# Kernel tuning notes

Hardware: AMD Instinct MI355X
Metric: run time of the kernel (lower is better)

Reference implementation:

```python
import jax, jax.numpy as jnp
import numpy as np

B, F, D, V = 8192, 26, 32, 100000
H1, H2 = 128, 128  # cin_size
U1, U2 = 400, 400  # dnn hidden units


def setup_inputs() -> dict:
    key = jax.random.key(0)
    ks = jax.random.split(key, 12)
    s = 0.05  # keep activations/sigmoid in a sane range
    return {
        "dense_inputs": jax.random.normal(ks[0], (B, 13), jnp.float32),
        "sparse_inputs": jax.random.randint(ks[1], (B, F), 0, V, jnp.int32),
        "E": jax.random.normal(ks[2], (F, V, D), jnp.float32) * s,
        "W_cin0": jax.random.normal(ks[3], (F, F, H1), jnp.float32) * s,
        "W_cin1": jax.random.normal(ks[4], (F, H1, H2), jnp.float32) * s,
        "W1": jax.random.normal(ks[5], (F * D, U1), jnp.float32) * s,
        "b1": jnp.zeros((U1,), jnp.float32),
        "W2": jax.random.normal(ks[6], (U1, U2), jnp.float32) * s,
        "b2": jnp.zeros((U2,), jnp.float32),
        "w_lin": jax.random.normal(ks[7], (F, 1), jnp.float32) * s,
        "b_lin": jnp.zeros((1,), jnp.float32),
        "w_out": jax.random.normal(ks[8], (1 + H1 + H2 + U2 + 13, 1), jnp.float32) * s,
        "b_out": jnp.zeros((1,), jnp.float32),
    }


def reference(dense_inputs, sparse_inputs, E, W_cin0, W_cin1, W1, b1, W2, b2,
              w_lin, b_lin, w_out, b_out):
    # Linear part: Dense(1) applied to raw (cast) sparse ids, as in the TF code.
    linear_out = sparse_inputs.astype(jnp.float32) @ w_lin + b_lin  # [B,1]

    # Embedding lookup: per-field tables. embed[b,f,:] = E[f, sparse[b,f], :]
    embed = E[jnp.arange(F)[None, :], sparse_inputs]  # [B,F,D]

    # CIN. The split->matmul->reshape->conv1d chain is exactly:
    #   x_{k+1}[b,h,d] = sum_{i,j} W_k[i,j,h] * X0[b,i,d] * x_k[b,j,d]
    X0 = embed
    x1 = jnp.einsum('bid,bjd,ijh->bhd', X0, X0, W_cin0)   # [B,H1,D]
    x2 = jnp.einsum('bid,bjd,ijh->bhd', X0, x1, W_cin1)   # [B,H2,D]
    cin_out = jnp.concatenate([x1, x2], axis=1).sum(axis=-1)  # [B,H1+H2]

    # DNN on flattened embeddings (dropout rate 0 -> identity at inference).
    v = embed.reshape(B, F * D)
    h = jax.nn.relu(v @ W1 + b1)
    h = jax.nn.relu(h @ W2 + b2)  # [B,U2]

    total = jnp.concatenate([linear_out, cin_out, h, dense_inputs], axis=-1)
    return jax.nn.sigmoid(total @ w_out + b_out)  # [B,1]
```

## Files before the change

kernel.cpp:

```cpp
#include <hip/hip_runtime.h>
#include <hip/hip_bf16.h>
#include <math.h>

typedef __attribute__((ext_vector_type(8))) short bf16x8;
typedef __attribute__((ext_vector_type(4))) float f32x4;

#define B_ 8192
#define F_ 26
#define D_ 32
#define V_ 100000
#define NP_ 351
#define KP_ 352

static const size_t OFF_VB   = 0;
static const size_t OFF_FD0  = 13631488;
static const size_t OFF_PDH2 = 13664256;
static const size_t OFF_H1B  = 13795328;
static const size_t OFF_W0T  = 20348928;
static const size_t OFF_W1T  = 20439040;
static const size_t OFF_W2T  = 21104640;
static const size_t OFF_MWT  = 21424640;

static __device__ __forceinline__ unsigned short f2b(float f) {
    unsigned int u = __float_as_uint(f);
    return (unsigned short)((u + 0x7FFF + ((u >> 16) & 1)) >> 16);
}
static __device__ __forceinline__ unsigned short f2bt(float f) {
    return (unsigned short)(__float_as_uint(f) >> 16);
}
static __device__ __forceinline__ unsigned int pk2t(float a, float b) {
    return __builtin_amdgcn_perm(__float_as_uint(b), __float_as_uint(a), 0x07060302u);
}
static __device__ __forceinline__ float bf2f(unsigned short u) {
    return __uint_as_float(((unsigned int)u) << 16);
}

static __device__ __forceinline__ void transpose_body(
    const float* __restrict__ src, unsigned short* __restrict__ dst,
    int K, int N, int bx, int by)
{
    __shared__ float tl[32][33];
    const int lx = threadIdx.x & 31, ly = threadIdx.x >> 5;
    const int n0 = bx * 32, k0 = by * 32;
#pragma unroll
    for (int i = 0; i < 4; ++i) {
        int k = k0 + ly + i * 8, n = n0 + lx;
        if (k < K && n < N) tl[ly + i * 8][lx] = src[(size_t)k * N + n];
    }
    __syncthreads();
#pragma unroll
    for (int i = 0; i < 4; ++i) {
        int n = n0 + ly + i * 8, k = k0 + lx;
        if (k < K && n < N) dst[(size_t)n * K + k] = f2b(tl[lx][ly + i * 8]);
    }
}

__global__ __launch_bounds__(256) void k0_all(
    const float* __restrict__ W0, const float* __restrict__ Wc1,
    const float* __restrict__ W1, const float* __restrict__ W2,
    const float* __restrict__ wout,
    unsigned short* __restrict__ W0t, unsigned short* __restrict__ W1t,
    unsigned short* __restrict__ W2t, float* __restrict__ Mwt)
{
    int bid = blockIdx.x;
    if (bid < 176) {
        int g = bid * 256 + threadIdx.x;
        if (g < 128 * KP_) {
            int h = g / KP_, p = g % KP_;
            float w = 0.f;
            if (p < NP_) {
                int i = 0, base = 0;
                while (base + (F_ - i) <= p) { base += F_ - i; ++i; }
                int j = i + (p - base);
                w = W0[(i * F_ + j) * 128 + h];
                if (i != j) w += W0[(j * F_ + i) * 128 + h];
            }
            W0t[g] = f2b(w);
        }
        return;
    }
    bid -= 176;
    if (bid < 338) { transpose_body(W1, W1t, 832, 400, bid % 13, bid / 13); return; }
    bid -= 338;
    if (bid < 169) { transpose_body(W2, W2t, 400, 400, bid % 13, bid / 13); return; }
    bid -= 169;
    {
        int g = bid * 256 + threadIdx.x;
        if (g < 128 * 32) {
            int j = g >> 5, i = g & 31;
            float s = 0.f;
            if (i < F_) {
                const float* row = Wc1 + ((size_t)i * 128 + j) * 128;
                for (int h = 0; h < 128; ++h) s = fmaf(row[h], wout[129 + h], s);
            }
            Mwt[g] = s;
        }
    }
}

__global__ __launch_bounds__(256) void k1_embed_cin(
    const int*   __restrict__ sparse,
    const float* __restrict__ E,
    const unsigned short* __restrict__ W0t,
    const float* __restrict__ wlin,
    const float* __restrict__ blin,
    const float* __restrict__ wout,
    const float* __restrict__ Mwt,
    unsigned short* __restrict__ vb,
    float* __restrict__ fdot0)
{
    __shared__ __align__(16) unsigned short embB[64][40];
    __shared__ __align__(16) unsigned short Pbuf[64 * 360];
    __shared__ float wdot[4];
    __shared__ float linv[52];
    __shared__ int   idxs[52];
    __shared__ unsigned char pI[NP_], pJ[NP_];

    const int b0 = blockIdx.x * 2, t = threadIdx.x;

    if (t < 52) {
        int bb = t >= 26 ? 1 : 0, ff = t - bb * 26;
        int id = sparse[(b0 + bb) * F_ + ff];
        idxs[t] = id;
        linv[t] = (float)id * wlin[ff];
    }
    if (t < F_) {
        int i = t, base = F_ * i - (i * (i - 1)) / 2;
        for (int j = i; j < F_; ++j) { pI[base + j - i] = (unsigned char)i; pJ[base + j - i] = (unsigned char)j; }
    }
    __syncthreads();

    for (int r = t; r < 416; r += 256) {
        int f = r >> 3, q = r & 7;
        int bb = f >= 26 ? 1 : 0, ff = f - bb * 26;
        float4 v4 = *(const float4*)(E + ((size_t)ff * V_ + idxs[f]) * D_ + q * 4);
        uint2 uu; uu.x = pk2t(v4.x, v4.y); uu.y = pk2t(v4.z, v4.w);
        *(uint2*)&embB[bb * 32 + ff][q * 4] = uu;
        *(uint2*)(vb + (size_t)(b0 + bb) * 832 + ff * 32 + q * 4) = uu;
    }
    if (t < 192) {
        int row = t >> 4, bb = row >= 6 ? 1 : 0, rr = row - bb * 6;
        *(unsigned int*)&embB[bb * 32 + 26 + rr][(t & 15) * 2] = 0u;
    }
    __syncthreads();

    {
        const int d = t & 31, sub = t >> 5;
        const int bb = sub & 1, pb = sub >> 1;
        const int e0 = bb * 32;
        const int p0 = pb * 88;
        unsigned short* Prow = &Pbuf[(e0 + d) * 360];
        for (int k = 0; k < 44; ++k) {
            int p = p0 + 2 * k;
            float a = bf2f(embB[e0 + pI[p]][d]) * bf2f(embB[e0 + pJ[p]][d]);
            float c = (p + 1 < NP_) ? bf2f(embB[e0 + pI[p + 1]][d]) * bf2f(embB[e0 + pJ[p + 1]][d]) : 0.f;
            *(unsigned int*)&Prow[p] = pk2t(a, c);
        }
    }
    __syncthreads();

    const int wave = t >> 6, lane = t & 63;
    const int lr = lane & 15, lg = lane >> 4;
    const int bb = wave & 1;
    const int h0 = (wave >> 1) * 64;
    f32x4 acc[2][4] = {};
    {
        const unsigned short* Ab = &Pbuf[(bb * 32 + lr) * 360];
        const unsigned short* Bb = W0t + (size_t)(h0 + lr) * KP_ + lg * 8;
        for (int kt = 0; kt < 11; ++kt) {
            const int ko = kt * 32 + lg * 8;
            bf16x8 a0 = *(const bf16x8*)(Ab + ko);
            bf16x8 a1 = *(const bf16x8*)(Ab + 16 * 360 + ko);
#pragma unroll
            for (int n = 0; n < 4; ++n) {
                bf16x8 bw = *(const bf16x8*)(Bb + (size_t)(n * 16) * KP_ + kt * 32);
                acc[0][n] = __builtin_amdgcn_mfma_f32_16x16x32_bf16(a0, bw, acc[0][n], 0, 0, 0);
                acc[1][n] = __builtin_amdgcn_mfma_f32_16x16x32_bf16(a1, bw, acc[1][n], 0, 0, 0);
            }
        }
    }

    float dotv = 0.f;
#pragma unroll
    for (int n = 0; n < 4; ++n) {
        float s = acc[0][n][0] + acc[0][n][1] + acc[0][n][2] + acc[0][n][3]
                + acc[1][n][0] + acc[1][n][1] + acc[1][n][2] + acc[1][n][3];
        s += __shfl_xor(s, 16, 64);
        s += __shfl_xor(s, 32, 64);
        if (lg == 0) dotv += s * wout[1 + h0 + n * 16 + lr];
    }
    __syncthreads();

#pragma unroll
    for (int n = 0; n < 4; ++n) {
        const int base = ((bb << 7) + h0 + n * 16 + lr) * 40;
#pragma unroll
        for (int mi = 0; mi < 2; ++mi) {
            *(unsigned int*)&Pbuf[base + mi * 16 + lg * 4]     = pk2t(acc[mi][n][0], acc[mi][n][1]);
            *(unsigned int*)&Pbuf[base + mi * 16 + lg * 4 + 2] = pk2t(acc[mi][n][2], acc[mi][n][3]);
        }
    }
    __syncthreads();

    {
        bf16x8 ga0 = *(const bf16x8*)&embB[bb * 32 + lr][lg * 8];
        bf16x8 ga1 = *(const bf16x8*)&embB[bb * 32 + 16 + lr][lg * 8];
#pragma unroll
        for (int n = 0; n < 4; ++n) {
            const int j = h0 + n * 16 + lr;
            bf16x8 xb = *(const bf16x8*)&Pbuf[((bb << 7) + j) * 40 + lg * 8];
            f32x4 g0 = {}, g1 = {};
            g0 = __builtin_amdgcn_mfma_f32_16x16x32_bf16(ga0, xb, g0, 0, 0, 0);
            g1 = __builtin_amdgcn_mfma_f32_16x16x32_bf16(ga1, xb, g1, 0, 0, 0);
            const float* mr = Mwt + j * 32;
            float4 m0 = *(const float4*)(mr + lg * 4);
            float4 m1 = *(const float4*)(mr + 16 + lg * 4);
            dotv += g0[0] * m0.x + g0[1] * m0.y + g0[2] * m0.z + g0[3] * m0.w
                  + g1[0] * m1.x + g1[1] * m1.y + g1[2] * m1.z + g1[3] * m1.w;
        }
    }
#pragma unroll
    for (int off = 1; off <= 32; off <<= 1) dotv += __shfl_xor(dotv, off, 64);
    if (lane == 0) wdot[wave] = dotv;
    __syncthreads();

    if (t < 2) {
        float s = blin[0];
        for (int f = 0; f < F_; ++f) s += linv[t * 26 + f];
        fdot0[b0 + t] = s * wout[0] + wdot[t] + wdot[t + 2];
    }
}

static __device__ __forceinline__ void gemm_core(
    const unsigned short* __restrict__ A, int lda,
    const unsigned short* __restrict__ Bt, int ldb, int N,
    int m0, int n0, int kbase, int kend,
    unsigned short (*As)[40], unsigned short (*Bs)[40],
    f32x4 (*acc)[2])
{
    const int t = threadIdx.x;
    const int wave = t >> 6, lane = t & 63;
    const int lr = lane & 15, lg = lane >> 4;
    const int wn = wave * 32;
    const int ar = t >> 2, kg = (t & 3) * 8;

    const unsigned short* aptr = A  + (size_t)(m0 + ar) * lda + kbase + kg;
    const unsigned short* bp0  = Bt + (size_t)(n0 + ar) * ldb + kbase + kg;
    const unsigned short* bp1  = Bt + (size_t)(n0 + 64 + ar) * ldb + kbase + kg;
    const bool bn0 = (n0 + ar) < N, bn1 = (n0 + 64 + ar) < N;
    const uint4 z4 = make_uint4(0u, 0u, 0u, 0u);
    const int nkt = (kend - kbase + 31) >> 5;
    uint4 av, bv0, bv1;
    {
        int k = kbase + kg;
        av  = (k < kend)        ? *(const uint4*)aptr : z4;
        bv0 = (bn0 && k < kend) ? *(const uint4*)bp0  : z4;
        bv1 = (bn1 && k < kend) ? *(const uint4*)bp1  : z4;
    }
    for (int kt = 0; kt < nkt; ++kt) {
        *(uint4*)&As[ar][kg]      = av;
        *(uint4*)&Bs[ar][kg]      = bv0;
        *(uint4*)&Bs[64 + ar][kg] = bv1;
        __syncthreads();
        if (kt + 1 < nkt) {
            int kn = kbase + (kt + 1) * 32 + kg;
            av  = (kn < kend)        ? *(const uint4*)(aptr + (kt + 1) * 32) : z4;
            bv0 = (bn0 && kn < kend) ? *(const uint4*)(bp0  + (kt + 1) * 32) : z4;
            bv1 = (bn1 && kn < kend) ? *(const uint4*)(bp1  + (kt + 1) * 32) : z4;
        }
        bf16x8 af[4], bfr[2];
#pragma unroll
        for (int i = 0; i < 4; ++i) af[i]  = *(const bf16x8*)&As[i * 16 + lr][lg * 8];
#pragma unroll
        for (int j = 0; j < 2; ++j) bfr[j] = *(const bf16x8*)&Bs[wn + j * 16 + lr][lg * 8];
#pragma unroll
        for (int i = 0; i < 4; ++i)
#pragma unroll
            for (int j = 0; j < 2; ++j)
                acc[i][j] = __builtin_amdgcn_mfma_f32_16x16x32_bf16(af[i], bfr[j], acc[i][j], 0, 0, 0);
        __syncthreads();
    }
}

__global__ __launch_bounds__(256) void k2_h1(
    const unsigned short* __restrict__ vb, const unsigned short* __restrict__ W1t,
    const float* __restrict__ b1, unsigned short* __restrict__ h1b)
{
    __shared__ __align__(16) unsigned short As[64][40];
    __shared__ __align__(16) unsigned short Bs[128][40];
    const int t = threadIdx.x;
    const int wave = t >> 6, lane = t & 63;
    const int lr = lane & 15, lg = lane >> 4;
    const int m0 = blockIdx.y * 64, n0 = blockIdx.x * 128;
    f32x4 acc[4][2] = {};
    gemm_core(vb, 832, W1t, 832, 400, m0, n0, 0, 832, As, Bs, acc);
#pragma unroll
    for (int i = 0; i < 4; ++i) {
        int mrow = m0 + i * 16 + lg * 4;
#pragma unroll
        for (int j = 0; j < 2; ++j) {
            int col = n0 + wave * 32 + j * 16 + lr;
            if (col >= 400) continue;
            float bb = b1[col];
#pragma unroll
            for (int r = 0; r < 4; ++r)
                h1b[(size_t)(mrow + r) * 400 + col] = f2bt(fmaxf(acc[i][j][r] + bb, 0.f));
        }
    }
}

__global__ __launch_bounds__(256) void k2_h2(
    const unsigned short* __restrict__ h1b, const unsigned short* __restrict__ W2t,
    const float* __restrict__ b2, const float* __restrict__ wout,
    float* __restrict__ pdh2)
{
    __shared__ __align__(16) unsigned short As[64][40];
    __shared__ __align__(16) unsigned short Bs[128][40];
    __shared__ float red[4][64];
    const int t = threadIdx.x;
    const int wave = t >> 6, lane = t & 63;
    const int lr = lane & 15, lg = lane >> 4;
    const int m0 = blockIdx.y * 64, n0 = blockIdx.x * 128;
    f32x4 acc[4][2] = {};
    gemm_core(h1b, 400, W2t, 400, 400, m0, n0, 0, 400, As, Bs, acc);
    float v[4][4];
#pragma unroll
    for (int i = 0; i < 4; ++i)
#pragma unroll
        for (int r = 0; r < 4; ++r) {
            float s = 0.f;
#pragma unroll
            for (int j = 0; j < 2; ++j) {
                int col = n0 + wave * 32 + j * 16 + lr;
                if (col < 400)
                    s = fmaf(fmaxf(acc[i][j][r] + b2[col], 0.f), wout[257 + col], s);
            }
#pragma unroll
            for (int off = 1; off <= 8; off <<= 1) s += __shfl_xor(s, off, 64);
            v[i][r] = s;
        }
    if (lr == 0) {
#pragma unroll
        for (int i = 0; i < 4; ++i)
#pragma unroll
            for (int r = 0; r < 4; ++r) red[wave][i * 16 + lg * 4 + r] = v[i][r];
    }
    __syncthreads();
    if (t < 64) pdh2[(size_t)blockIdx.x * B_ + m0 + t] = red[0][t] + red[1][t] + red[2][t] + red[3][t];
}

__global__ __launch_bounds__(256) void k3_final(
    const float* __restrict__ fdot0,
    const float* __restrict__ pdh2,
    const float* __restrict__ dense,
    const float* __restrict__ wout,
    const float* __restrict__ bout,
    float* __restrict__ out)
{
    const int b = blockIdx.x * 256 + threadIdx.x;
    float s = fdot0[b];
#pragma unroll
    for (int z = 0; z < 4; ++z) s += pdh2[(size_t)z * B_ + b];
#pragma unroll
    for (int q = 0; q < 13; ++q) s = fmaf(dense[(size_t)b * 13 + q], wout[657 + q], s);
    out[b] = 1.f / (1.f + expf(-(s + bout[0])));
}

extern "C" void kernel_launch(void* const* d_in, const int* in_sizes, int n_in,
                              void* d_out, int out_size, void* d_ws, size_t ws_size,
                              hipStream_t stream) {
    const float* dense  = (const float*)d_in[0];
    const int*   sparse = (const int*)  d_in[1];
    const float* E      = (const float*)d_in[2];
    const float* W0     = (const float*)d_in[3];
    const float* Wc1    = (const float*)d_in[4];
    const float* W1     = (const float*)d_in[5];
    const float* b1     = (const float*)d_in[6];
    const float* W2     = (const float*)d_in[7];
    const float* b2     = (const float*)d_in[8];
    const float* wlin   = (const float*)d_in[9];
    const float* blin   = (const float*)d_in[10];
    const float* wout   = (const float*)d_in[11];
    const float* bout   = (const float*)d_in[12];
    float* out = (float*)d_out;

    char* ws = (char*)d_ws;
    unsigned short* vb    = (unsigned short*)(ws + OFF_VB);
    float*          fdot0 = (float*)(ws + OFF_FD0);
    float*          pdh2  = (float*)(ws + OFF_PDH2);
    unsigned short* h1b   = (unsigned short*)(ws + OFF_H1B);
    unsigned short* W0t   = (unsigned short*)(ws + OFF_W0T);
    unsigned short* W1t   = (unsigned short*)(ws + OFF_W1T);
    unsigned short* W2t   = (unsigned short*)(ws + OFF_W2T);
    float*          Mwt   = (float*)(ws + OFF_MWT);

    k0_all<<<176 + 338 + 169 + 16, 256, 0, stream>>>(W0, Wc1, W1, W2, wout, W0t, W1t, W2t, Mwt);
    k1_embed_cin<<<B_ / 2, 256, 0, stream>>>(sparse, E, W0t, wlin, blin, wout, Mwt, vb, fdot0);
    k2_h1<<<dim3(4, 128), 256, 0, stream>>>(vb, W1t, b1, h1b);
    k2_h2<<<dim3(4, 128), 256, 0, stream>>>(h1b, W2t, b2, wout, pdh2);
    k3_final<<<B_ / 256, 256, 0, stream>>>(fdot0, pdh2, dense, wout, bout, out);
}
```

Measured before the change: 525.2 us.

## Fold CIN weights into a precomputed pairwise kernel and simplify per-sample CIN

Result: faster. 491.3 us (-6.5%).

```diff
diff --git a/kernel.cpp b/kernel.cpp
--- a/kernel.cpp
+++ b/kernel.cpp
@@ -9,17 +9,15 @@
 #define F_ 26
 #define D_ 32
 #define V_ 100000
-#define NP_ 351
-#define KP_ 352
 
 static const size_t OFF_VB   = 0;
 static const size_t OFF_FD0  = 13631488;
 static const size_t OFF_PDH2 = 13664256;
 static const size_t OFF_H1B  = 13795328;
-static const size_t OFF_W0T  = 20348928;
-static const size_t OFF_W1T  = 20439040;
-static const size_t OFF_W2T  = 21104640;
-static const size_t OFF_MWT  = 21424640;
+static const size_t OFF_W1T  = 20348928;
+static const size_t OFF_W2T  = 21014528;
+static const size_t OFF_MTF  = 21334528;
+static const size_t OFF_K2T  = 21350912;
 
 static __device__ __forceinline__ unsigned short f2b(float f) {
     unsigned int u = __float_as_uint(f);
@@ -55,180 +53,152 @@
     }
 }
 
-__global__ __launch_bounds__(256) void k0_all(
-    const float* __restrict__ W0, const float* __restrict__ Wc1,
+__global__ __launch_bounds__(256) void k0a(
     const float* __restrict__ W1, const float* __restrict__ W2,
-    const float* __restrict__ wout,
-    unsigned short* __restrict__ W0t, unsigned short* __restrict__ W1t,
-    unsigned short* __restrict__ W2t, float* __restrict__ Mwt)
-{
+    const float* __restrict__ Wc1, const float* __restrict__ wout,
+    unsigned short* __restrict__ W1t, unsigned short* __restrict__ W2t,
+    float* __restrict__ MtF)
+{
+    __shared__ float w2s[128];
     int bid = blockIdx.x;
-    if (bid < 176) {
-        int g = bid * 256 + threadIdx.x;
-        if (g < 128 * KP_) {
-            int h = g / KP_, p = g % KP_;
-            float w = 0.f;
-            if (p < NP_) {
-                int i = 0, base = 0;
-                while (base + (F_ - i) <= p) { base += F_ - i; ++i; }
-                int j = i + (p - base);
-                w = W0[(i * F_ + j) * 128 + h];
-                if (i != j) w += W0[(j * F_ + i) * 128 + h];
-            }
-            W0t[g] = f2b(w);
-        }
-        return;
-    }
-    bid -= 176;
     if (bid < 338) { transpose_body(W1, W1t, 832, 400, bid % 13, bid / 13); return; }
     bid -= 338;
     if (bid < 169) { transpose_body(W2, W2t, 400, 400, bid % 13, bid / 13); return; }
     bid -= 169;
-    {
-        int g = bid * 256 + threadIdx.x;
-        if (g < 128 * 32) {
-            int j = g >> 5, i = g & 31;
-            float s = 0.f;
-            if (i < F_) {
-                const float* row = Wc1 + ((size_t)i * 128 + j) * 128;
-                for (int h = 0; h < 128; ++h) s = fmaf(row[h], wout[129 + h], s);
+    if (threadIdx.x < 128) w2s[threadIdx.x] = wout[129 + threadIdx.x];
+    __syncthreads();
+    int g = bid * 256 + threadIdx.x;
+    int i = g >> 7, j = g & 127;
+    float s = 0.f;
+    if (i < F_) {
+        const float* row = Wc1 + ((size_t)i * 128 + j) * 128;
+        for (int h = 0; h < 128; h += 4) {
+            float4 a = *(const float4*)(row + h);
+            s = fmaf(a.x, w2s[h], s);
+            s = fmaf(a.y, w2s[h + 1], s);
+            s = fmaf(a.z, w2s[h + 2], s);
+            s = fmaf(a.w, w2s[h + 3], s);
+        }
+    } else if (i == F_) {
+        s = wout[1 + j];
+    }
+    MtF[g] = s;
+}
+
+__global__ __launch_bounds__(256) void k0b(
+    const float* __restrict__ W0, const float* __restrict__ MtF,
+    unsigned short* __restrict__ K2T)
+{
+    int g = blockIdx.x * 256 + threadIdx.x;
+    int q = g >> 5, i = g & 31;
+    float s = 0.f;
+    if (q < 351) {
+        int a = 0, base = 0;
+        while (base + (F_ - a) <= q) { base += F_ - a; ++a; }
+        int b = a + (q - base);
+        const float* r0 = W0 + ((size_t)a * F_ + b) * 128;
+        const float* r1 = W0 + ((size_t)b * F_ + a) * 128;
+        const float* m  = MtF + (size_t)i * 128;
+        if (a == b) {
+            for (int j = 0; j < 128; j += 4) {
+                float4 w = *(const float4*)(r0 + j);
+                float4 mm = *(const float4*)(m + j);
+                s += w.x * mm.x + w.y * mm.y + w.z * mm.z + w.w * mm.w;
             }
-            Mwt[g] = s;
-        }
-    }
+        } else {
+            for (int j = 0; j < 128; j += 4) {
+                float4 w = *(const float4*)(r0 + j);
+                float4 w1 = *(const float4*)(r1 + j);
+                float4 mm = *(const float4*)(m + j);
+                s += (w.x + w1.x) * mm.x + (w.y + w1.y) * mm.y
+                   + (w.z + w1.z) * mm.z + (w.w + w1.w) * mm.w;
+            }
+        }
+    }
+    unsigned short hi = f2b(s);
+    float lo = s - bf2f(hi);
+    K2T[g] = hi;
+    K2T[11264 + g] = f2b(lo);
 }
 
 __global__ __launch_bounds__(256) void k1_embed_cin(
     const int*   __restrict__ sparse,
     const float* __restrict__ E,
-    const unsigned short* __restrict__ W0t,
+    const unsigned short* __restrict__ K2T,
     const float* __restrict__ wlin,
     const float* __restrict__ blin,
     const float* __restrict__ wout,
-    const float* __restrict__ Mwt,
     unsigned short* __restrict__ vb,
     float* __restrict__ fdot0)
 {
-    __shared__ __align__(16) unsigned short embB[64][40];
-    __shared__ __align__(16) unsigned short Pbuf[64 * 360];
-    __shared__ float wdot[4];
-    __shared__ float linv[52];
-    __shared__ int   idxs[52];
-    __shared__ unsigned char pI[NP_], pJ[NP_];
-
-    const int b0 = blockIdx.x * 2, t = threadIdx.x;
-
-    if (t < 52) {
-        int bb = t >= 26 ? 1 : 0, ff = t - bb * 26;
-        int id = sparse[(b0 + bb) * F_ + ff];
+    __shared__ __align__(16) unsigned short embT[32][40];
+    __shared__ unsigned int PQ[352];
+    __shared__ int idxs[F_];
+    __shared__ float red[4];
+
+    const int b = blockIdx.x, t = threadIdx.x;
+    float cind = 0.f;
+
+    if (t < F_) {
+        int id = sparse[b * F_ + t];
         idxs[t] = id;
-        linv[t] = (float)id * wlin[ff];
-    }
-    if (t < F_) {
-        int i = t, base = F_ * i - (i * (i - 1)) / 2;
-        for (int j = i; j < F_; ++j) { pI[base + j - i] = (unsigned char)i; pJ[base + j - i] = (unsigned char)j; }
-    }
-    __syncthreads();
-
-    for (int r = t; r < 416; r += 256) {
-        int f = r >> 3, q = r & 7;
-        int bb = f >= 26 ? 1 : 0, ff = f - bb * 26;
-        float4 v4 = *(const float4*)(E + ((size_t)ff * V_ + idxs[f]) * D_ + q * 4);
+        cind = (float)id * wlin[t] * wout[0];
+        int base = F_ * t - (t * (t - 1)) / 2;
+        for (int j = t; j < F_; ++j)
+            PQ[base + j - t] = (unsigned)t | ((unsigned)j << 16);
+    }
+    if (t == F_) PQ[351] = 0u;
+    if (t >= 32 && t < 64) {
+        int d = t - 32;
+        embT[d][26] = 0x3F80;
+        embT[d][27] = 0; embT[d][28] = 0; embT[d][29] = 0;
+        embT[d][30] = 0; embT[d][31] = 0;
+    }
+    __syncthreads();
+
+    if (t < 208) {
+        int f = t >> 3, q = t & 7;
+        float4 v4 = *(const float4*)(E + ((size_t)f * V_ + idxs[f]) * D_ + q * 4);
         uint2 uu; uu.x = pk2t(v4.x, v4.y); uu.y = pk2t(v4.z, v4.w);
-        *(uint2*)&embB[bb * 32 + ff][q * 4] = uu;
-        *(uint2*)(vb + (size_t)(b0 + bb) * 832 + ff * 32 + q * 4) = uu;
-    }
-    if (t < 192) {
-        int row = t >> 4, bb = row >= 6 ? 1 : 0, rr = row - bb * 6;
-        *(unsigned int*)&embB[bb * 32 + 26 + rr][(t & 15) * 2] = 0u;
-    }
-    __syncthreads();
-
-    {
-        const int d = t & 31, sub = t >> 5;
-        const int bb = sub & 1, pb = sub >> 1;
-        const int e0 = bb * 32;
-        const int p0 = pb * 88;
-        unsigned short* Prow = &Pbuf[(e0 + d) * 360];
-        for (int k = 0; k < 44; ++k) {
-            int p = p0 + 2 * k;
-            float a = bf2f(embB[e0 + pI[p]][d]) * bf2f(embB[e0 + pJ[p]][d]);
-            float c = (p + 1 < NP_) ? bf2f(embB[e0 + pI[p + 1]][d]) * bf2f(embB[e0 + pJ[p + 1]][d]) : 0.f;
-            *(unsigned int*)&Prow[p] = pk2t(a, c);
-        }
+        *(uint2*)(vb + (size_t)b * 832 + f * 32 + q * 4) = uu;
+        embT[q * 4 + 0][f] = f2bt(v4.x);
+        embT[q * 4 + 1][f] = f2bt(v4.y);
+        embT[q * 4 + 2][f] = f2bt(v4.z);
+        embT[q * 4 + 3][f] = f2bt(v4.w);
     }
     __syncthreads();
 
     const int wave = t >> 6, lane = t & 63;
     const int lr = lane & 15, lg = lane >> 4;
-    const int bb = wave & 1;
-    const int h0 = (wave >> 1) * 64;
-    f32x4 acc[2][4] = {};
-    {
-        const unsigned short* Ab = &Pbuf[(bb * 32 + lr) * 360];
-        const unsigned short* Bb = W0t + (size_t)(h0 + lr) * KP_ + lg * 8;
-        for (int kt = 0; kt < 11; ++kt) {
-            const int ko = kt * 32 + lg * 8;
-            bf16x8 a0 = *(const bf16x8*)(Ab + ko);
-            bf16x8 a1 = *(const bf16x8*)(Ab + 16 * 360 + ko);
-#pragma unroll
-            for (int n = 0; n < 4; ++n) {
-                bf16x8 bw = *(const bf16x8*)(Bb + (size_t)(n * 16) * KP_ + kt * 32);
-                acc[0][n] = __builtin_amdgcn_mfma_f32_16x16x32_bf16(a0, bw, acc[0][n], 0, 0, 0);
-                acc[1][n] = __builtin_amdgcn_mfma_f32_16x16x32_bf16(a1, bw, acc[1][n], 0, 0, 0);
-            }
-        }
-    }
-
-    float dotv = 0.f;
-#pragma unroll
-    for (int n = 0; n < 4; ++n) {
-        float s = acc[0][n][0] + acc[0][n][1] + acc[0][n][2] + acc[0][n][3]
-                + acc[1][n][0] + acc[1][n][1] + acc[1][n][2] + acc[1][n][3];
-        s += __shfl_xor(s, 16, 64);
-        s += __shfl_xor(s, 32, 64);
-        if (lg == 0) dotv += s * wout[1 + h0 + n * 16 + lr];
-    }
-    __syncthreads();
-
-#pragma unroll
-    for (int n = 0; n < 4; ++n) {
-        const int base = ((bb << 7) + h0 + n * 16 + lr) * 40;
-#pragma unroll
-        for (int mi = 0; mi < 2; ++mi) {
-            *(unsigned int*)&Pbuf[base + mi * 16 + lg * 4]     = pk2t(acc[mi][n][0], acc[mi][n][1]);
-            *(unsigned int*)&Pbuf[base + mi * 16 + lg * 4 + 2] = pk2t(acc[mi][n][2], acc[mi][n][3]);
-        }
-    }
-    __syncthreads();
-
-    {
-        bf16x8 ga0 = *(const bf16x8*)&embB[bb * 32 + lr][lg * 8];
-        bf16x8 ga1 = *(const bf16x8*)&embB[bb * 32 + 16 + lr][lg * 8];
-#pragma unroll
-        for (int n = 0; n < 4; ++n) {
-            const int j = h0 + n * 16 + lr;
-            bf16x8 xb = *(const bf16x8*)&Pbuf[((bb << 7) + j) * 40 + lg * 8];
-            f32x4 g0 = {}, g1 = {};
-            g0 = __builtin_amdgcn_mfma_f32_16x16x32_bf16(ga0, xb, g0, 0, 0, 0);
-            g1 = __builtin_amdgcn_mfma_f32_16x16x32_bf16(ga1, xb, g1, 0, 0, 0);
-            const float* mr = Mwt + j * 32;
-            float4 m0 = *(const float4*)(mr + lg * 4);
-            float4 m1 = *(const float4*)(mr + 16 + lg * 4);
-            dotv += g0[0] * m0.x + g0[1] * m0.y + g0[2] * m0.z + g0[3] * m0.w
-                  + g1[0] * m1.x + g1[1] * m1.y + g1[2] * m1.z + g1[3] * m1.w;
-        }
-    }
-#pragma unroll
-    for (int off = 1; off <= 32; off <<= 1) dotv += __shfl_xor(dotv, off, 64);
-    if (lane == 0) wdot[wave] = dotv;
-    __syncthreads();
-
-    if (t < 2) {
-        float s = blin[0];
-        for (int f = 0; f < F_; ++f) s += linv[t * 26 + f];
-        fdot0[b0 + t] = s * wout[0] + wdot[t] + wdot[t + 2];
-    }
+    const int mt = wave & 1;
+    const int nb = wave >> 1;
+    bf16x8 af = *(const bf16x8*)&embT[mt * 16 + lr][lg * 8];
+    const unsigned short* ebase = &embT[mt * 16 + lg * 4][0];
+    const unsigned short* Kb = K2T + (size_t)lr * 32 + lg * 8;
+
+#pragma unroll
+    for (int s = 0; s < 11; ++s) {
+        const int nt = 2 * s + nb;
+        bf16x8 bh = *(const bf16x8*)(Kb + (size_t)nt * 512);
+        bf16x8 bl = *(const bf16x8*)(Kb + 11264 + (size_t)nt * 512);
+        f32x4 h = {};
+        h = __builtin_amdgcn_mfma_f32_16x16x32_bf16(af, bl, h, 0, 0, 0);
+        h = __builtin_amdgcn_mfma_f32_16x16x32_bf16(af, bh, h, 0, 0, 0);
+        unsigned pq = PQ[nt * 16 + lr];
+        int oi = (int)(pq & 0xFFFFu), oj = (int)(pq >> 16);
+#pragma unroll
+        for (int r = 0; r < 4; ++r) {
+            float ei = bf2f(ebase[r * 40 + oi]);
+            float ej = bf2f(ebase[r * 40 + oj]);
+            cind = fmaf(ei * ej, h[r], cind);
+        }
+    }
+
+#pragma unroll
+    for (int off = 1; off <= 32; off <<= 1) cind += __shfl_xor(cind, off, 64);
+    if (lane == 0) red[wave] = cind;
+    __syncthreads();
+    if (t == 0) fdot0[b] = red[0] + red[1] + red[2] + red[3] + blin[0] * wout[0];
 }
 
 static __device__ __forceinline__ void gemm_core(
@@ -389,13 +359,14 @@
     float*          fdot0 = (float*)(ws + OFF_FD0);
     float*          pdh2  = (float*)(ws + OFF_PDH2);
     unsigned short* h1b   = (unsigned short*)(ws + OFF_H1B);
-    unsigned short* W0t   = (unsigned short*)(ws + OFF_W0T);
     unsigned short* W1t   = (unsigned short*)(ws + OFF_W1T);
     unsigned short* W2t   = (unsigned short*)(ws + OFF_W2T);
-    float*          Mwt   = (float*)(ws + OFF_MWT);
-
-    k0_all<<<176 + 338 + 169 + 16, 256, 0, stream>>>(W0, Wc1, W1, W2, wout, W0t, W1t, W2t, Mwt);
-    k1_embed_cin<<<B_ / 2, 256, 0, stream>>>(sparse, E, W0t, wlin, blin, wout, Mwt, vb, fdot0);
+    float*          MtF   = (float*)(ws + OFF_MTF);
+    unsigned short* K2T   = (unsigned short*)(ws + OFF_K2T);
+
+    k0a<<<338 + 169 + 16, 256, 0, stream>>>(W1, W2, Wc1, wout, W1t, W2t, MtF);
+    k0b<<<44, 256, 0, stream>>>(W0, MtF, K2T);
+    k1_embed_cin<<<B_, 256, 0, stream>>>(sparse, E, K2T, wlin, blin, wout, vb, fdot0);
     k2_h1<<<dim3(4, 128), 256, 0, stream>>>(vb, W1t, b1, h1b);
     k2_h2<<<dim3(4, 128), 256, 0, stream>>>(h1b, W2t, b2, wout, pdh2);
     k3_final<<<B_ / 256, 256, 0, stream>>>(fdot0, pdh2, dense, wout, bout, out);
```
